# Performance work log

Measured on AMD Instinct MI355X. Metric: run time of the kernel, lower is better.

## Reference

```python
import jax, jax.numpy as jnp
import numpy as np

N_NODES = 100000
N_EDGES = 3200000
IN_FEAT = 128
HIDDEN = 128
CLASSES = 32


def gcn_conv(x, edge_index, W, b, n_nodes):
    """PyG GCNConv: linear -> symmetric-normalized scatter-add with self-loops -> +bias."""
    src, dst = edge_index[0], edge_index[1]
    loop = jnp.arange(n_nodes, dtype=edge_index.dtype)
    src = jnp.concatenate([src, loop])
    dst = jnp.concatenate([dst, loop])
    # degree (with self-loops) on destination nodes
    deg = jax.ops.segment_sum(jnp.ones_like(dst, dtype=x.dtype), dst, num_segments=n_nodes)
    dinv = jnp.where(deg > 0, jax.lax.rsqrt(deg), 0.0)
    norm = dinv[src] * dinv[dst]  # [E+N]
    h = x @ W  # [N, out]
    msg = h[src] * norm[:, None]  # gather + scale, [E+N, out]
    out = jax.ops.segment_sum(msg, dst, num_segments=n_nodes)  # scatter-add
    return out + b


def setup_inputs() -> dict:
    key = jax.random.key(0)
    k1, k2, k3, k4 = jax.random.split(key, 4)
    x = jax.random.normal(k1, (N_NODES, IN_FEAT), dtype=jnp.float32)
    edge_index = jax.random.randint(k2, (2, N_EDGES), 0, N_NODES, dtype=jnp.int64)
    W1 = jax.random.normal(k3, (IN_FEAT, HIDDEN), dtype=jnp.float32) / np.sqrt(IN_FEAT)
    b1 = jnp.zeros((HIDDEN,), dtype=jnp.float32)
    W2 = jax.random.normal(k4, (HIDDEN, CLASSES), dtype=jnp.float32) / np.sqrt(HIDDEN)
    b2 = jnp.zeros((CLASSES,), dtype=jnp.float32)
    return {"x": x, "edge_index": edge_index, "W1": W1, "b1": b1, "W2": W2, "b2": b2}


def reference(x, edge_index, W1, b1, W2, b2):
    n = x.shape[0]
    h = gcn_conv(x, edge_index, W1, b1, n)
    h = jax.nn.relu(h)
    # dropout p=0.5 is identity in eval mode
    out = gcn_conv(h, edge_index, W2, b2, n)
    return out
```

## Files before the change

### kernel.cpp

```cpp
#include <hip/hip_runtime.h>

#define N_NODES 100000
#define N_EDGES 3200000
#define F_IN 128
#define F_HID 128
#define F_OUT 32
#define CAP 96

#define NBUCK 391
#define CAPB 8960
#define EPT 32

#define BM 64
#define BK 16
#define XPAD 68

typedef float f32x2 __attribute__((ext_vector_type(2)));

__device__ inline unsigned pack_bf16(float a, float b) {
    unsigned ua = __float_as_uint(a);
    ua = (ua + 0x7fffu + ((ua >> 16) & 1u)) >> 16;
    unsigned ub = __float_as_uint(b);
    ub = (ub + 0x7fffu + ((ub >> 16) & 1u)) >> 16;
    return ua | (ub << 16);
}
__device__ inline float lo16(unsigned u) { return __uint_as_float(u << 16); }
__device__ inline float hi16(unsigned u) { return __uint_as_float(u & 0xffff0000u); }

__global__ __launch_bounds__(256) void k_part(const int* __restrict__ ei,
                                              int* __restrict__ gcur,
                                              unsigned* __restrict__ stage) {
    __shared__ int cnt[NBUCK];
    __shared__ int base[NBUCK];
    int tid = threadIdx.x;
    for (int i = tid; i < NBUCK; i += 256) cnt[i] = 0;
    __syncthreads();

    long e0 = (long)blockIdx.x * (256 * EPT);
#pragma unroll 4
    for (int i = 0; i < EPT; ++i) {
        long e = e0 + i * 256 + tid;
        if (e < N_EDGES) atomicAdd(&cnt[ei[N_EDGES + e] >> 8], 1);
    }
    __syncthreads();
    for (int i = tid; i < NBUCK; i += 256) {
        base[i] = atomicAdd(&gcur[i], cnt[i]);
        cnt[i] = 0;
    }
    __syncthreads();
#pragma unroll 4
    for (int i = 0; i < EPT; ++i) {
        long e = e0 + i * 256 + tid;
        if (e < N_EDGES) {
            int s = ei[e];
            int d = ei[N_EDGES + e];
            int b = d >> 8;
            int pos = base[b] + atomicAdd(&cnt[b], 1);
            if (pos < CAPB)
                stage[(size_t)b * CAPB + pos] = ((unsigned)(d & 255) << 17) | (unsigned)s;
        }
    }
}

__global__ __launch_bounds__(256) void k_csr(const unsigned* __restrict__ stage,
                                             const int* __restrict__ gcur,
                                             int* __restrict__ csr,
                                             int* __restrict__ deg,
                                             float* __restrict__ dinv) {
    __shared__ int cnt[256];
    int b = blockIdx.x;
    int tid = threadIdx.x;
    cnt[tid] = 0;
    __syncthreads();

    int d0 = b << 8;
    int m = gcur[b];
    if (m > CAPB) m = CAPB;
    const unsigned* sp = stage + (size_t)b * CAPB;
    for (int i = tid; i < m; i += 256) {
        unsigned rec = __builtin_nontemporal_load(sp + i);
        int s = (int)(rec & 0x1ffffu);
        int dl = (int)(rec >> 17);
        int pos = atomicAdd(&cnt[dl], 1);
        if (pos < CAP) csr[(size_t)(d0 + dl) * CAP + pos] = s;
    }
    __syncthreads();
    int dd = d0 + tid;
    if (dd < N_NODES) {
        int dg = cnt[tid];
        deg[dd] = dg;
        dinv[dd] = rsqrtf((float)(dg + 1));
    }
}

__global__ __launch_bounds__(256) void k_gemm1(const float* __restrict__ x,
                                               const float* __restrict__ W1,
                                               const float* __restrict__ dinv,
                                               unsigned* __restrict__ g1u) {
    __shared__ float xT[BK][XPAD];
    __shared__ float wt[BK][F_HID];

    int tid = threadIdx.x;
    int m0 = blockIdx.x * BM;

    int rg = tid >> 4;
    int cg = tid & 15;
    int r0 = rg * 4;
    int c0 = cg * 8;

    int lr = tid >> 2;
    int lk = (tid & 3) * 4;
    int gr = m0 + lr;
    int grc = gr < N_NODES ? gr : N_NODES - 1;
    const float* xrow = x + (size_t)grc * F_IN + lk;

    float acc[4][8];
#pragma unroll
    for (int i = 0; i < 4; ++i)
#pragma unroll
        for (int j = 0; j < 8; ++j) acc[i][j] = 0.f;

    for (int k0 = 0; k0 < F_IN; k0 += BK) {
        float4 v = *(const float4*)(xrow + k0);
        const float4* w4 = (const float4*)(W1 + (size_t)k0 * F_HID);
        float4 wv0 = w4[tid];
        float4 wv1 = w4[tid + 256];

        xT[lk + 0][lr] = v.x;
        xT[lk + 1][lr] = v.y;
        xT[lk + 2][lr] = v.z;
        xT[lk + 3][lr] = v.w;
        ((float4*)wt)[tid] = wv0;
        ((float4*)wt)[tid + 256] = wv1;
        __syncthreads();

#pragma unroll
        for (int k = 0; k < BK; ++k) {
            float a[4], b[8];
            *(float4*)a = *(const float4*)&xT[k][r0];
            *(float4*)(b + 0) = *(const float4*)&wt[k][c0];
            *(float4*)(b + 4) = *(const float4*)&wt[k][c0 + 4];
#pragma unroll
            for (int i = 0; i < 4; ++i)
#pragma unroll
                for (int j = 0; j < 8; ++j)
                    acc[i][j] = fmaf(a[i], b[j], acc[i][j]);
        }
        __syncthreads();
    }

#pragma unroll
    for (int i = 0; i < 4; ++i) {
        int n = m0 + r0 + i;
        if (n < N_NODES) {
            float s = dinv[n];
            uint4 o;
            o.x = pack_bf16(acc[i][0] * s, acc[i][1] * s);
            o.y = pack_bf16(acc[i][2] * s, acc[i][3] * s);
            o.z = pack_bf16(acc[i][4] * s, acc[i][5] * s);
            o.w = pack_bf16(acc[i][6] * s, acc[i][7] * s);
            *(uint4*)(g1u + (size_t)n * 64 + (c0 >> 1)) = o;
        }
    }
}

__global__ __launch_bounds__(256) void k_pull1_gemm2(const int* __restrict__ csr,
                                                     const int* __restrict__ deg_i,
                                                     const unsigned* __restrict__ g1u,
                                                     const float* __restrict__ dinv,
                                                     const float* __restrict__ b1,
                                                     const float* __restrict__ W2,
                                                     unsigned* __restrict__ g2u) {
    __shared__ float w2l[F_HID * F_OUT];
    __shared__ float al[4][F_HID];
    {
        const float4* w4 = (const float4*)W2;
        float4* wl4 = (float4*)w2l;
#pragma unroll
        for (int i = 0; i < 4; ++i)
            wl4[threadIdx.x + i * 256] = w4[threadIdx.x + i * 256];
    }
    int lane = threadIdx.x & 63;
    int wv = threadIdx.x >> 6;
    int n = __builtin_amdgcn_readfirstlane(blockIdx.x * 4 + wv);

    int deg = deg_i[n];
    if (deg > CAP) deg = CAP;
    const int* crow = csr + (size_t)n * CAP;
    int sidx0 = __builtin_nontemporal_load(crow + lane);
    int sidx1 = __builtin_nontemporal_load(crow + 64 + (lane & 31));

    f32x2 ac0, ac1, ac2, ac3;
    {
        unsigned us = g1u[(size_t)n * 64 + lane];
        ac0 = (f32x2){lo16(us), hi16(us)};
        ac1 = (f32x2){0.f, 0.f}; ac2 = ac1; ac3 = ac1;
    }

#define GATHER(S, ACC)                                            \
    {                                                             \
        const unsigned* p = g1u + ((size_t)(unsigned)(S) << 6);   \
        unsigned v = p[lane];                                     \
        ACC += (f32x2){lo16(v), hi16(v)};                         \
    }

    int m1 = deg < 64 ? deg : 64;
    int j = 0;
    for (; j + 3 < m1; j += 4) {
        int s0 = __builtin_amdgcn_readlane(sidx0, j);
        int s1 = __builtin_amdgcn_readlane(sidx0, j + 1);
        int s2 = __builtin_amdgcn_readlane(sidx0, j + 2);
        int s3 = __builtin_amdgcn_readlane(sidx0, j + 3);
        GATHER(s0, ac0) GATHER(s1, ac1) GATHER(s2, ac2) GATHER(s3, ac3)
    }
    for (; j < m1; ++j) {
        int s0 = __builtin_amdgcn_readlane(sidx0, j);
        GATHER(s0, ac0)
    }
    int m2 = deg - 64;
    for (j = 0; j + 3 < m2; j += 4) {
        int s0 = __builtin_amdgcn_readlane(sidx1, j);
        int s1 = __builtin_amdgcn_readlane(sidx1, j + 1);
        int s2 = __builtin_amdgcn_readlane(sidx1, j + 2);
        int s3 = __builtin_amdgcn_readlane(sidx1, j + 3);
        GATHER(s0, ac0) GATHER(s1, ac1) GATHER(s2, ac2) GATHER(s3, ac3)
    }
    for (; j < m2; ++j) {
        int s0 = __builtin_amdgcn_readlane(sidx1, j);
        GATHER(s0, ac0)
    }
#undef GATHER

    f32x2 a = (ac0 + ac1) + (ac2 + ac3);

    float di = dinv[n];
    float2 bb = *(const float2*)(b1 + lane * 2);
    float a0 = fmaxf(fmaf(di, a.x, bb.x), 0.f);
    float a1 = fmaxf(fmaf(di, a.y, bb.y), 0.f);
    *(float2*)(&al[wv][lane * 2]) = make_float2(a0, a1);
    __syncthreads();

    int jj = lane & 31, kh = lane >> 5;
    float sum = 0.f;
#pragma unroll
    for (int kk = 0; kk < 64; ++kk) {
        int k = kh * 64 + kk;
        sum = fmaf(al[wv][k], w2l[k * F_OUT + jj], sum);
    }
    sum += __shfl_xor(sum, 32);
    float sv = sum * di;
    int fl16 = lane & 15;
    float sa = __shfl(sv, fl16 * 2);
    float sb = __shfl(sv, fl16 * 2 + 1);
    if (lane < 16) g2u[(size_t)n * 16 + fl16] = pack_bf16(sa, sb);
}

__global__ __launch_bounds__(256) void k_pull2(const int* __restrict__ csr,
                                               const int* __restrict__ deg_i,
                                               const unsigned* __restrict__ g2u,
                                               const float* __restrict__ dinv,
                                               const float* __restrict__ b2,
                                               float* __restrict__ out) {
    int lane = threadIdx.x & 63;
    int wv = threadIdx.x >> 6;
    int n = __builtin_amdgcn_readfirstlane(blockIdx.x * 4 + wv);
    int fl = lane & 15, eq = lane >> 4;

    int deg = deg_i[n];
    if (deg > CAP) deg = CAP;
    const int* crow = csr + (size_t)n * CAP;

    f32x2 acc = {0.f, 0.f}, acc2 = {0.f, 0.f};
    for (int e0 = 0; e0 < deg; e0 += 8) {
        int ip0 = e0 + eq, ip1 = e0 + 4 + eq;
        bool ok0 = ip0 < deg, ok1 = ip1 < deg;
        int s0 = ok0 ? __builtin_nontemporal_load(crow + ip0) : 0;
        int s1 = ok1 ? __builtin_nontemporal_load(crow + ip1) : 0;
        unsigned v0 = ok0 ? g2u[(unsigned)s0 * 16u + fl] : 0u;
        unsigned v1 = ok1 ? g2u[(unsigned)s1 * 16u + fl] : 0u;
        acc += (f32x2){lo16(v0), hi16(v0)};
        acc2 += (f32x2){lo16(v1), hi16(v1)};
    }
    acc += acc2;
    acc.x += __shfl_xor(acc.x, 32);
    acc.y += __shfl_xor(acc.y, 32);
    acc.x += __shfl_xor(acc.x, 16);
    acc.y += __shfl_xor(acc.y, 16);

    if (eq == 0) {
        unsigned us = g2u[(size_t)n * 16 + fl];
        float di = dinv[n];
        float2 bb = *(const float2*)(b2 + fl * 2);
        f32x2 o;
        o.x = fmaf(di, acc.x + lo16(us), bb.x);
        o.y = fmaf(di, acc.y + hi16(us), bb.y);
        __builtin_nontemporal_store(o, (f32x2*)(out + (size_t)n * F_OUT + fl * 2));
    }
}

extern "C" void kernel_launch(void* const* d_in, const int* in_sizes, int n_in,
                              void* d_out, int out_size, void* d_ws, size_t ws_size,
                              hipStream_t stream) {
    const float* x  = (const float*)d_in[0];
    const int*   ei = (const int*)d_in[1];
    const float* W1 = (const float*)d_in[2];
    const float* b1 = (const float*)d_in[3];
    const float* W2 = (const float*)d_in[4];
    const float* b2 = (const float*)d_in[5];
    float* out = (float*)d_out;

    char* ws = (char*)d_ws;
    int*      deg   = (int*)(ws);
    float*    dinv  = (float*)(ws + 524288);
    int*      gcur  = (int*)(ws + 1048576);
    int*      csr   = (int*)(ws + 1572864);
    unsigned* stage = (unsigned*)(ws + 40000000);
    unsigned* g1u   = (unsigned*)(ws + 54016000);
    unsigned* g2u   = (unsigned*)(ws + 79616000);

    (void)hipMemsetAsync(gcur, 0, 4096, stream);
    k_part<<<(N_EDGES + 256 * EPT - 1) / (256 * EPT), 256, 0, stream>>>(ei, gcur, stage);
    k_csr<<<NBUCK, 256, 0, stream>>>(stage, gcur, csr, deg, dinv);

    k_gemm1<<<(N_NODES + BM - 1) / BM, 256, 0, stream>>>(x, W1, dinv, g1u);

    k_pull1_gemm2<<<N_NODES / 4, 256, 0, stream>>>(csr, deg, g1u, dinv, b1, W2, g2u);
    k_pull2<<<N_NODES / 4, 256, 0, stream>>>(csr, deg, g2u, dinv, b2, out);
}
```

Baseline: 341.0 us.

## Remap layer-2 pull to one node per 16-lane group and widen layer-1 gather unroll

k_pull2 now assigns one node to each 16-lane quarter-wave, so a 256-thread block covers 16 nodes. Each group broadcasts neighbor indices with width-16 shuffles and accumulates with four independent chains, which removes the cross-quarter shuffle reduction and the idle lanes in the final store. k_pull1 unrolls its gather by 8 with more accumulators to keep more loads in flight, and it only loads the second index chunk when degree exceeds 64. The cost is higher register pressure, plus divergence between nodes of different degree inside one wave in pull2.

```diff
diff --git a/kernel.cpp b/kernel.cpp
--- a/kernel.cpp
+++ b/kernel.cpp
@@ -187,14 +187,14 @@
     int deg = deg_i[n];
     if (deg > CAP) deg = CAP;
     const int* crow = csr + (size_t)n * CAP;
-    int sidx0 = __builtin_nontemporal_load(crow + lane);
-    int sidx1 = __builtin_nontemporal_load(crow + 64 + (lane & 31));
-
-    f32x2 ac0, ac1, ac2, ac3;
+    int sidx0 = (lane < deg) ? __builtin_nontemporal_load(crow + lane) : 0;
+
+    f32x2 ac0, ac1, ac2, ac3, ac4, ac5, ac6, ac7;
     {
         unsigned us = g1u[(size_t)n * 64 + lane];
         ac0 = (f32x2){lo16(us), hi16(us)};
-        ac1 = (f32x2){0.f, 0.f}; ac2 = ac1; ac3 = ac1;
+        ac1 = (f32x2){0.f, 0.f};
+        ac2 = ac1; ac3 = ac1; ac4 = ac1; ac5 = ac1; ac6 = ac1; ac7 = ac1;
     }
 
 #define GATHER(S, ACC)                                            \
@@ -206,32 +206,33 @@
 
     int m1 = deg < 64 ? deg : 64;
     int j = 0;
-    for (; j + 3 < m1; j += 4) {
+    for (; j + 7 < m1; j += 8) {
         int s0 = __builtin_amdgcn_readlane(sidx0, j);
         int s1 = __builtin_amdgcn_readlane(sidx0, j + 1);
         int s2 = __builtin_amdgcn_readlane(sidx0, j + 2);
         int s3 = __builtin_amdgcn_readlane(sidx0, j + 3);
+        int s4 = __builtin_amdgcn_readlane(sidx0, j + 4);
+        int s5 = __builtin_amdgcn_readlane(sidx0, j + 5);
+        int s6 = __builtin_amdgcn_readlane(sidx0, j + 6);
+        int s7 = __builtin_amdgcn_readlane(sidx0, j + 7);
         GATHER(s0, ac0) GATHER(s1, ac1) GATHER(s2, ac2) GATHER(s3, ac3)
+        GATHER(s4, ac4) GATHER(s5, ac5) GATHER(s6, ac6) GATHER(s7, ac7)
     }
     for (; j < m1; ++j) {
         int s0 = __builtin_amdgcn_readlane(sidx0, j);
         GATHER(s0, ac0)
     }
-    int m2 = deg - 64;
-    for (j = 0; j + 3 < m2; j += 4) {
-        int s0 = __builtin_amdgcn_readlane(sidx1, j);
-        int s1 = __builtin_amdgcn_readlane(sidx1, j + 1);
-        int s2 = __builtin_amdgcn_readlane(sidx1, j + 2);
-        int s3 = __builtin_amdgcn_readlane(sidx1, j + 3);
-        GATHER(s0, ac0) GATHER(s1, ac1) GATHER(s2, ac2) GATHER(s3, ac3)
-    }
-    for (; j < m2; ++j) {
-        int s0 = __builtin_amdgcn_readlane(sidx1, j);
-        GATHER(s0, ac0)
+    if (deg > 64) {
+        int sidx1 = __builtin_nontemporal_load(crow + 64 + (lane & 31));
+        int m2 = deg - 64;
+        for (j = 0; j < m2; ++j) {
+            int s0 = __builtin_amdgcn_readlane(sidx1, j);
+            GATHER(s0, ac0)
+        }
     }
 #undef GATHER
 
-    f32x2 a = (ac0 + ac1) + (ac2 + ac3);
+    f32x2 a = ((ac0 + ac1) + (ac2 + ac3)) + ((ac4 + ac5) + (ac6 + ac7));
 
     float di = dinv[n];
     float2 bb = *(const float2*)(b1 + lane * 2);
@@ -263,39 +264,49 @@
                                                float* __restrict__ out) {
     int lane = threadIdx.x & 63;
     int wv = threadIdx.x >> 6;
-    int n = __builtin_amdgcn_readfirstlane(blockIdx.x * 4 + wv);
-    int fl = lane & 15, eq = lane >> 4;
-
+    int qw = lane >> 4, fl = lane & 15;
+    int n = blockIdx.x * 16 + wv * 4 + qw;
+
+    unsigned u0 = g2u[(size_t)n * 16 + fl];
+    float a0x = lo16(u0), a0y = hi16(u0);
+    float a1x = 0.f, a1y = 0.f, a2x = 0.f, a2y = 0.f, a3x = 0.f, a3y = 0.f;
     int deg = deg_i[n];
     if (deg > CAP) deg = CAP;
     const int* crow = csr + (size_t)n * CAP;
-
-    f32x2 acc = {0.f, 0.f}, acc2 = {0.f, 0.f};
-    for (int e0 = 0; e0 < deg; e0 += 8) {
-        int ip0 = e0 + eq, ip1 = e0 + 4 + eq;
-        bool ok0 = ip0 < deg, ok1 = ip1 < deg;
-        int s0 = ok0 ? __builtin_nontemporal_load(crow + ip0) : 0;
-        int s1 = ok1 ? __builtin_nontemporal_load(crow + ip1) : 0;
-        unsigned v0 = ok0 ? g2u[(unsigned)s0 * 16u + fl] : 0u;
-        unsigned v1 = ok1 ? g2u[(unsigned)s1 * 16u + fl] : 0u;
-        acc += (f32x2){lo16(v0), hi16(v0)};
-        acc2 += (f32x2){lo16(v1), hi16(v1)};
-    }
-    acc += acc2;
-    acc.x += __shfl_xor(acc.x, 32);
-    acc.y += __shfl_xor(acc.y, 32);
-    acc.x += __shfl_xor(acc.x, 16);
-    acc.y += __shfl_xor(acc.y, 16);
-
-    if (eq == 0) {
-        unsigned us = g2u[(size_t)n * 16 + fl];
-        float di = dinv[n];
-        float2 bb = *(const float2*)(b2 + fl * 2);
-        f32x2 o;
-        o.x = fmaf(di, acc.x + lo16(us), bb.x);
-        o.y = fmaf(di, acc.y + hi16(us), bb.y);
-        __builtin_nontemporal_store(o, (f32x2*)(out + (size_t)n * F_OUT + fl * 2));
-    }
+    for (int e0 = 0; e0 < deg; e0 += 16) {
+        int rem = deg - e0;
+        int m = rem < 16 ? rem : 16;
+        int sidx = (fl < m) ? __builtin_nontemporal_load(crow + e0 + fl) : 0;
+        int j = 0;
+        for (; j + 3 < m; j += 4) {
+            int s0 = __shfl(sidx, j, 16);
+            int s1 = __shfl(sidx, j + 1, 16);
+            int s2 = __shfl(sidx, j + 2, 16);
+            int s3 = __shfl(sidx, j + 3, 16);
+            unsigned v0 = g2u[(unsigned)s0 * 16u + fl];
+            unsigned v1 = g2u[(unsigned)s1 * 16u + fl];
+            unsigned v2 = g2u[(unsigned)s2 * 16u + fl];
+            unsigned v3 = g2u[(unsigned)s3 * 16u + fl];
+            a0x += lo16(v0); a0y += hi16(v0);
+            a1x += lo16(v1); a1y += hi16(v1);
+            a2x += lo16(v2); a2y += hi16(v2);
+            a3x += lo16(v3); a3y += hi16(v3);
+        }
+        for (; j < m; ++j) {
+            int s0 = __shfl(sidx, j, 16);
+            unsigned v0 = g2u[(unsigned)s0 * 16u + fl];
+            a0x += lo16(v0); a0y += hi16(v0);
+        }
+    }
+    float ax = (a0x + a1x) + (a2x + a3x);
+    float ay = (a0y + a1y) + (a2y + a3y);
+
+    float di = dinv[n];
+    float2 bb = *(const float2*)(b2 + fl * 2);
+    f32x2 o;
+    o.x = fmaf(di, ax, bb.x);
+    o.y = fmaf(di, ay, bb.y);
+    __builtin_nontemporal_store(o, (f32x2*)(out + (size_t)n * F_OUT + fl * 2));
 }
 
 extern "C" void kernel_launch(void* const* d_in, const int* in_sizes, int n_in,
@@ -325,5 +336,5 @@
     k_gemm1<<<(N_NODES + BM - 1) / BM, 256, 0, stream>>>(x, W1, dinv, g1u);
 
     k_pull1_gemm2<<<N_NODES / 4, 256, 0, stream>>>(csr, deg, g1u, dinv, b1, W2, g2u);
-    k_pull2<<<N_NODES / 4, 256, 0, stream>>>(csr, deg, g2u, dinv, b2, out);
-}
+    k_pull2<<<N_NODES / 16, 256, 0, stream>>>(csr, deg, g2u, dinv, b2, out);
+}
```

Result: faster. 295.8 us (-13.3%).
